# Kernel optimization log

Measured on AMD Instinct MI355X. Metric: run time of the kernel, lower is better.

Reference implementation:

```python
import jax, jax.numpy as jnp
import numpy as np

N = 10000  # num_users + num_posts


def gcn_conv(x, edge_index, W, b):
    """PyG-style GCNConv: out = D^-1/2 (A+I) D^-1/2 (x W) + b."""
    h = x @ W  # [N, d]
    src, dst = edge_index[0], edge_index[1]
    loop = jnp.arange(N, dtype=src.dtype)
    src = jnp.concatenate([src, loop])
    dst = jnp.concatenate([dst, loop])
    ones = jnp.ones(src.shape[0], dtype=h.dtype)
    deg = jax.ops.segment_sum(ones, dst, num_segments=N)  # in-degree incl. self-loop
    dinv = jnp.where(deg > 0, jax.lax.rsqrt(deg), 0.0)
    norm = dinv[src] * dinv[dst]  # [E+N]
    msg = h[src] * norm[:, None]  # gather + scale
    out = jax.ops.segment_sum(msg, dst, num_segments=N)  # scatter-add
    return out + b


def setup_inputs() -> dict:
    key = jax.random.key(0)
    k1, k2, k3, k4 = jax.random.split(key, 4)
    E = 320000
    H = 64
    x = jax.random.normal(k1, (N, N), dtype=jnp.float32)
    edge_index = jax.random.randint(k2, (2, E), 0, N, dtype=jnp.int64)
    W1 = jax.random.normal(k3, (N, H), dtype=jnp.float32) / np.sqrt(N)
    b1 = jnp.zeros((H,), dtype=jnp.float32)
    W2 = jax.random.normal(k4, (H, H), dtype=jnp.float32) / np.sqrt(H)
    b2 = jnp.zeros((H,), dtype=jnp.float32)
    return {"x": x, "edge_index": edge_index, "W1": W1, "b1": b1, "W2": W2, "b2": b2}


def reference(x, edge_index, W1, b1, W2, b2):
    h = gcn_conv(x, edge_index, W1, b1)
    h = jax.nn.relu(h)
    return gcn_conv(h, edge_index, W2, b2)
```

## Files before the change

### kernel.cpp

```cpp
#include <hip/hip_runtime.h>
#include <hip/hip_bf16.h>

#define NND 10000
#define HD 64
#define KPAD 10112
#define ROWS 64
#define RBLK 157
#define NCHUNK 3
#define KCHUNK 3456
#define KSTEP 128
#define KHEAD 5632
#define CAP 96
#define ABYTES 32768
#define BBYTES 16384
#define BUFB (ABYTES + BBYTES)

typedef __attribute__((ext_vector_type(8))) short bf16x8;
typedef __attribute__((ext_vector_type(4))) float f32x4;

__device__ __forceinline__ short f2bf(float f) {
    unsigned u = __builtin_bit_cast(unsigned, f);
    u += 0x7FFFu + ((u >> 16) & 1u);
    return (short)(u >> 16);
}

__device__ __forceinline__ void gload16(const void* gp, void* lp) {
    __builtin_amdgcn_global_load_lds(
        (const __attribute__((address_space(1))) unsigned int*)gp,
        (__attribute__((address_space(3))) unsigned int*)lp, 16, 0, 0);
}

__device__ __forceinline__ void gload16nt(const void* gp, void* lp) {
    __builtin_amdgcn_global_load_lds(
        (const __attribute__((address_space(1))) unsigned int*)gp,
        (__attribute__((address_space(3))) unsigned int*)lp, 16, 0, 2);
}

__global__ __launch_bounds__(256) void prep2_kernel(const float* __restrict__ W1,
        int* __restrict__ cnt, float* __restrict__ h, short* __restrict__ w1t) {
    __shared__ float tile[64][65];
    const int t = threadIdx.x;
    const int k0 = blockIdx.x * 64;
    #pragma unroll
    for (int i = 0; i < 16; ++i) {
        int r = i * 4 + (t >> 6);
        int c = t & 63;
        int k = k0 + r;
        tile[r][c] = (k < NND) ? W1[(size_t)k * HD + c] : 0.f;
    }
    __syncthreads();
    #pragma unroll
    for (int i = 0; i < 16; ++i) {
        int c = i * 4 + (t >> 6);
        int k = t & 63;
        if (k0 + k < KPAD)
            w1t[(size_t)c * KPAD + k0 + k] = f2bf(tile[k][c]);
    }
    int tid = blockIdx.x * 256 + t;
    if (tid < NND) cnt[tid] = 0;
    f32x4* h4 = (f32x4*)h;
    f32x4 z = {0.f, 0.f, 0.f, 0.f};
    #pragma unroll
    for (int i = 0; i < 4; ++i) {
        int idx = tid + i * 40448;
        if (idx < NND * HD / 4) h4[idx] = z;
    }
}

__global__ __launch_bounds__(256, 1) void csrgemm1_kernel(const float* __restrict__ x,
        const short* __restrict__ w1t, float* __restrict__ h,
        const int* __restrict__ ei, int* __restrict__ cnt, int* __restrict__ csr, int E) {
    __shared__ f32x4 smem4[3 * BUFB / 16];
    char* smem = (char*)smem4;
    const int l = threadIdx.x & 63;
    const int w = threadIdx.x >> 6;
    const int r0 = (blockIdx.x / NCHUNK) * ROWS;
    const int kstart = (blockIdx.x % NCHUNK) * KCHUNK;
    const int kend = min(KPAD, kstart + KCHUNK);
    const int nsteps = (kend - kstart) >> 7;

    const int wr = (w & 1) * 32;
    const int wc = (w >> 1) * 32;
    const int akg = l >> 4;
    const int l15 = l & 15;
    const int l7 = l & 7;

    f32x4 acc[2][2];
    #pragma unroll
    for (int i = 0; i < 2; ++i)
        #pragma unroll
        for (int j = 0; j < 2; ++j) acc[i][j] = f32x4{0.f, 0.f, 0.f, 0.f};

    union AFU { bf16x8 v; __hip_bfloat162 p[4]; };

    auto stage = [&](int buf, int k0) {
        char* sb = smem + buf * BUFB;
        const bool cached = (k0 < KHEAD);
        #pragma unroll
        for (int i = 0; i < 8; ++i) {
            int row = w * 16 + i * 2 + (l >> 5);
            int rg = r0 + row; if (rg >= NND) rg = 0;
            int pl = ((l & 31) >> 1) ^ (row & 7);
            const char* gp = (const char*)x + (size_t)rg * (NND * 4)
                             + (size_t)k0 * 4 + pl * 32 + (l & 1) * 16;
            if (k0 + pl * 8 + (l & 1) * 4 + 3 >= NND)
                gp = (const char*)x;
            if (cached) gload16(gp, sb + w * 8192 + i * 1024);
            else        gload16nt(gp, sb + w * 8192 + i * 1024);
        }
        #pragma unroll
        for (int j = 0; j < 4; ++j) {
            int col = w * 16 + j * 4 + (l >> 4);
            int cl = (l & 15) ^ (col & 7);
            const char* gp = (const char*)w1t + (size_t)col * (KPAD * 2)
                             + (size_t)k0 * 2 + cl * 16;
            gload16(gp, sb + ABYTES + w * 4096 + j * 1024);
        }
    };

    stage(0, kstart);
    if (nsteps > 1) stage(1, kstart + KSTEP);
    {
        const int tid = blockIdx.x * 256 + threadIdx.x;
        const int base = tid * 4;
        if (base < E) {
            if (((E & 3) == 0) && base + 4 <= E) {
                int4 sa = *(const int4*)(ei + base);
                int4 da = *(const int4*)(ei + E + base);
                int p0 = atomicAdd(&cnt[da.x], 1);
                int p1 = atomicAdd(&cnt[da.y], 1);
                int p2 = atomicAdd(&cnt[da.z], 1);
                int p3 = atomicAdd(&cnt[da.w], 1);
                if (p0 < CAP) csr[da.x * CAP + p0] = sa.x;
                if (p1 < CAP) csr[da.y * CAP + p1] = sa.y;
                if (p2 < CAP) csr[da.z * CAP + p2] = sa.z;
                if (p3 < CAP) csr[da.w * CAP + p3] = sa.w;
            } else {
                for (int e = base; e < E && e < base + 4; ++e) {
                    int s = ei[e], d = ei[E + e];
                    int pos = atomicAdd(&cnt[d], 1);
                    if (pos < CAP) csr[d * CAP + pos] = s;
                }
            }
        }
    }
    asm volatile("s_waitcnt vmcnt(0)" ::: "memory");
    for (int t = 0; t < nsteps; ++t) {
        if (t + 1 < nsteps) asm volatile("s_waitcnt vmcnt(12)" ::: "memory");
        else                asm volatile("s_waitcnt vmcnt(0)" ::: "memory");
        __builtin_amdgcn_s_barrier();
        if (t + 2 < nsteps) stage((t + 2) % 3, kstart + (t + 2) * KSTEP);
        const char* sb = smem + (t % 3) * BUFB;
        #pragma unroll
        for (int ks = 0; ks < 4; ++ks) {
            int cp = (ks * 4 + akg) ^ l7;
            #pragma unroll
            for (int rg = 0; rg < 2; ++rg) {
                int arow = wr + rg * 16 + l15;
                const char* ap = sb + arow * 512 + cp * 32;
                f32x4 a0 = *(const f32x4*)ap;
                f32x4 a1 = *(const f32x4*)(ap + 16);
                AFU af;
                af.p[0] = __float22bfloat162_rn(float2{a0[0], a0[1]});
                af.p[1] = __float22bfloat162_rn(float2{a0[2], a0[3]});
                af.p[2] = __float22bfloat162_rn(float2{a1[0], a1[1]});
                af.p[3] = __float22bfloat162_rn(float2{a1[2], a1[3]});
                #pragma unroll
                for (int cg = 0; cg < 2; ++cg) {
                    int col = wc + cg * 16 + l15;
                    bf16x8 b = *(const bf16x8*)(sb + ABYTES + col * 256 + cp * 16);
                    acc[rg][cg] = __builtin_amdgcn_mfma_f32_16x16x32_bf16(af.v, b, acc[rg][cg], 0, 0, 0);
                }
            }
        }
    }
    #pragma unroll
    for (int rg = 0; rg < 2; ++rg) {
        const int crow = r0 + wr + rg * 16 + akg * 4;
        #pragma unroll
        for (int cg = 0; cg < 2; ++cg) {
            const int ccol = wc + cg * 16 + l15;
            #pragma unroll
            for (int j = 0; j < 4; ++j) {
                int row = crow + j;
                if (row < NND)
                    unsafeAtomicAdd(&h[(size_t)row * HD + ccol], acc[rg][cg][j]);
            }
        }
    }
}

__global__ __launch_bounds__(256) void agg1g2_kernel(const float* __restrict__ h,
        const int* __restrict__ csr, const int* __restrict__ cnt,
        const float* __restrict__ b1, const float* __restrict__ W2,
        float* __restrict__ h2) {
    __shared__ float w2s[HD * HD];
    __shared__ float rowbuf[4][HD];
    for (int i = threadIdx.x; i < HD * HD; i += 256) w2s[i] = W2[i];
    const int wave = threadIdx.x >> 6, lane = threadIdx.x & 63;
    const int d = blockIdx.x * 4 + wave;
    const int n = min(cnt[d], CAP);
    const float dd = rsqrtf((float)(n + 1));
    float acc = fmaf(h[(size_t)d * HD + lane], dd * dd, b1[lane]);
    const int* row = csr + d * CAP;
    int j = 0;
    for (; j + 8 <= n; j += 8) {
        int s0 = row[j],   s1 = row[j+1], s2 = row[j+2], s3 = row[j+3];
        int s4 = row[j+4], s5 = row[j+5], s6 = row[j+6], s7 = row[j+7];
        acc = fmaf(h[(size_t)s0 * HD + lane], rsqrtf((float)(cnt[s0] + 1)) * dd, acc);
        acc = fmaf(h[(size_t)s1 * HD + lane], rsqrtf((float)(cnt[s1] + 1)) * dd, acc);
        acc = fmaf(h[(size_t)s2 * HD + lane], rsqrtf((float)(cnt[s2] + 1)) * dd, acc);
        acc = fmaf(h[(size_t)s3 * HD + lane], rsqrtf((float)(cnt[s3] + 1)) * dd, acc);
        acc = fmaf(h[(size_t)s4 * HD + lane], rsqrtf((float)(cnt[s4] + 1)) * dd, acc);
        acc = fmaf(h[(size_t)s5 * HD + lane], rsqrtf((float)(cnt[s5] + 1)) * dd, acc);
        acc = fmaf(h[(size_t)s6 * HD + lane], rsqrtf((float)(cnt[s6] + 1)) * dd, acc);
        acc = fmaf(h[(size_t)s7 * HD + lane], rsqrtf((float)(cnt[s7] + 1)) * dd, acc);
    }
    for (; j < n; ++j) {
        int s0 = row[j];
        acc = fmaf(h[(size_t)s0 * HD + lane], rsqrtf((float)(cnt[s0] + 1)) * dd, acc);
    }
    rowbuf[wave][lane] = fmaxf(acc, 0.f);
    __syncthreads();
    float s = 0.f;
    #pragma unroll
    for (int k = 0; k < HD; ++k)
        s = fmaf(rowbuf[wave][k], w2s[k * HD + lane], s);
    h2[(size_t)d * HD + lane] = s;
}

__global__ __launch_bounds__(256) void agg2_kernel(const float* __restrict__ feat,
        const int* __restrict__ csr, const int* __restrict__ cnt,
        const float* __restrict__ bias, float* __restrict__ out) {
    const int wave = threadIdx.x >> 6, lane = threadIdx.x & 63;
    const int d = blockIdx.x * 4 + wave;
    const int n = min(cnt[d], CAP);
    const float dd = rsqrtf((float)(n + 1));
    float acc = fmaf(feat[(size_t)d * HD + lane], dd * dd, bias[lane]);
    const int* row = csr + d * CAP;
    int j = 0;
    for (; j + 8 <= n; j += 8) {
        int s0 = row[j],   s1 = row[j+1], s2 = row[j+2], s3 = row[j+3];
        int s4 = row[j+4], s5 = row[j+5], s6 = row[j+6], s7 = row[j+7];
        acc = fmaf(feat[(size_t)s0 * HD + lane], rsqrtf((float)(cnt[s0] + 1)) * dd, acc);
        acc = fmaf(feat[(size_t)s1 * HD + lane], rsqrtf((float)(cnt[s1] + 1)) * dd, acc);
        acc = fmaf(feat[(size_t)s2 * HD + lane], rsqrtf((float)(cnt[s2] + 1)) * dd, acc);
        acc = fmaf(feat[(size_t)s3 * HD + lane], rsqrtf((float)(cnt[s3] + 1)) * dd, acc);
        acc = fmaf(feat[(size_t)s4 * HD + lane], rsqrtf((float)(cnt[s4] + 1)) * dd, acc);
        acc = fmaf(feat[(size_t)s5 * HD + lane], rsqrtf((float)(cnt[s5] + 1)) * dd, acc);
        acc = fmaf(feat[(size_t)s6 * HD + lane], rsqrtf((float)(cnt[s6] + 1)) * dd, acc);
        acc = fmaf(feat[(size_t)s7 * HD + lane], rsqrtf((float)(cnt[s7] + 1)) * dd, acc);
    }
    for (; j < n; ++j) {
        int s0 = row[j];
        acc = fmaf(feat[(size_t)s0 * HD + lane], rsqrtf((float)(cnt[s0] + 1)) * dd, acc);
    }
    out[(size_t)d * HD + lane] = acc;
}

extern "C" void kernel_launch(void* const* d_in, const int* in_sizes, int n_in,
                              void* d_out, int out_size, void* d_ws, size_t ws_size,
                              hipStream_t stream) {
    const float* x  = (const float*)d_in[0];
    const int*   ei = (const int*)d_in[1];
    const float* W1 = (const float*)d_in[2];
    const float* b1 = (const float*)d_in[3];
    const float* W2 = (const float*)d_in[4];
    const float* b2 = (const float*)d_in[5];
    float* out = (float*)d_out;
    const int E = in_sizes[1] / 2;

    char* ws = (char*)d_ws;
    int*   cnt  = (int*)(ws);
    float* h    = (float*)(ws + 40000);
    float* h2   = (float*)(ws + 2600000);
    short* w1t  = (short*)(ws + 5160000);
    int*   csr  = (int*)(ws + 6454336);

    prep2_kernel<<<158, 256, 0, stream>>>(W1, cnt, h, w1t);
    csrgemm1_kernel<<<RBLK * NCHUNK, 256, 0, stream>>>(x, w1t, h, ei, cnt, csr, E);
    agg1g2_kernel<<<2500, 256, 0, stream>>>(h, csr, cnt, b1, W2, h2);
    agg2_kernel<<<2500, 256, 0, stream>>>(h2, csr, cnt, b2, out);
}
```

Baseline: 138.4 us.

## Fold source-degree normalization into GEMM epilogue and move CSR build to prep

Builds the CSR adjacency and degree counts in the prep kernel, after a memset of the counts. This lets the GEMM epilogue scale each output row of x·W1 by its own inverse-sqrt degree, and the layer-1 aggregation likewise pre-scales h2. Both aggregation kernels then sum pre-scaled neighbor rows using four independent accumulators, with no per-neighbor count gather or rsqrt. In exchange, edge insertion no longer overlaps with the GEMM prologue loads, and there is an extra memset launch.

New measurement: 143.8 us. +3.9%, slower.

```diff
diff --git a/kernel.cpp b/kernel.cpp
--- a/kernel.cpp
+++ b/kernel.cpp
@@ -37,7 +37,8 @@
 }
 
 __global__ __launch_bounds__(256) void prep2_kernel(const float* __restrict__ W1,
-        int* __restrict__ cnt, float* __restrict__ h, short* __restrict__ w1t) {
+        int* __restrict__ cnt, float* __restrict__ h, short* __restrict__ w1t,
+        const int* __restrict__ ei, int* __restrict__ csr, int E) {
     __shared__ float tile[64][65];
     const int t = threadIdx.x;
     const int k0 = blockIdx.x * 64;
@@ -56,8 +57,7 @@
         if (k0 + k < KPAD)
             w1t[(size_t)c * KPAD + k0 + k] = f2bf(tile[k][c]);
     }
-    int tid = blockIdx.x * 256 + t;
-    if (tid < NND) cnt[tid] = 0;
+    const int tid = blockIdx.x * 256 + t;
     f32x4* h4 = (f32x4*)h;
     f32x4 z = {0.f, 0.f, 0.f, 0.f};
     #pragma unroll
@@ -65,11 +65,40 @@
         int idx = tid + i * 40448;
         if (idx < NND * HD / 4) h4[idx] = z;
     }
+    const int base = tid * 8;
+    if (base + 8 <= E) {
+        int4 sa = *(const int4*)(ei + base);
+        int4 sb = *(const int4*)(ei + base + 4);
+        int4 da = *(const int4*)(ei + E + base);
+        int4 db = *(const int4*)(ei + E + base + 4);
+        int p0 = atomicAdd(&cnt[da.x], 1);
+        int p1 = atomicAdd(&cnt[da.y], 1);
+        int p2 = atomicAdd(&cnt[da.z], 1);
+        int p3 = atomicAdd(&cnt[da.w], 1);
+        int p4 = atomicAdd(&cnt[db.x], 1);
+        int p5 = atomicAdd(&cnt[db.y], 1);
+        int p6 = atomicAdd(&cnt[db.z], 1);
+        int p7 = atomicAdd(&cnt[db.w], 1);
+        if (p0 < CAP) csr[da.x * CAP + p0] = sa.x;
+        if (p1 < CAP) csr[da.y * CAP + p1] = sa.y;
+        if (p2 < CAP) csr[da.z * CAP + p2] = sa.z;
+        if (p3 < CAP) csr[da.w * CAP + p3] = sa.w;
+        if (p4 < CAP) csr[db.x * CAP + p4] = sb.x;
+        if (p5 < CAP) csr[db.y * CAP + p5] = sb.y;
+        if (p6 < CAP) csr[db.z * CAP + p6] = sb.z;
+        if (p7 < CAP) csr[db.w * CAP + p7] = sb.w;
+    } else if (base < E) {
+        for (int e = base; e < E; ++e) {
+            int s = ei[e], d = ei[E + e];
+            int pos = atomicAdd(&cnt[d], 1);
+            if (pos < CAP) csr[d * CAP + pos] = s;
+        }
+    }
 }
 
 __global__ __launch_bounds__(256, 1) void csrgemm1_kernel(const float* __restrict__ x,
         const short* __restrict__ w1t, float* __restrict__ h,
-        const int* __restrict__ ei, int* __restrict__ cnt, int* __restrict__ csr, int E) {
+        const int* __restrict__ cnt) {
     __shared__ f32x4 smem4[3 * BUFB / 16];
     char* smem = (char*)smem4;
     const int l = threadIdx.x & 63;
@@ -120,31 +149,6 @@
 
     stage(0, kstart);
     if (nsteps > 1) stage(1, kstart + KSTEP);
-    {
-        const int tid = blockIdx.x * 256 + threadIdx.x;
-        const int base = tid * 4;
-        if (base < E) {
-            if (((E & 3) == 0) && base + 4 <= E) {
-                int4 sa = *(const int4*)(ei + base);
-                int4 da = *(const int4*)(ei + E + base);
-                int p0 = atomicAdd(&cnt[da.x], 1);
-                int p1 = atomicAdd(&cnt[da.y], 1);
-                int p2 = atomicAdd(&cnt[da.z], 1);
-                int p3 = atomicAdd(&cnt[da.w], 1);
-                if (p0 < CAP) csr[da.x * CAP + p0] = sa.x;
-                if (p1 < CAP) csr[da.y * CAP + p1] = sa.y;
-                if (p2 < CAP) csr[da.z * CAP + p2] = sa.z;
-                if (p3 < CAP) csr[da.w * CAP + p3] = sa.w;
-            } else {
-                for (int e = base; e < E && e < base + 4; ++e) {
-                    int s = ei[e], d = ei[E + e];
-                    int pos = atomicAdd(&cnt[d], 1);
-                    if (pos < CAP) csr[d * CAP + pos] = s;
-                }
-            }
-        }
-    }
-    asm volatile("s_waitcnt vmcnt(0)" ::: "memory");
     for (int t = 0; t < nsteps; ++t) {
         if (t + 1 < nsteps) asm volatile("s_waitcnt vmcnt(12)" ::: "memory");
         else                asm volatile("s_waitcnt vmcnt(0)" ::: "memory");
@@ -178,13 +182,15 @@
     for (int rg = 0; rg < 2; ++rg) {
         const int crow = r0 + wr + rg * 16 + akg * 4;
         #pragma unroll
-        for (int cg = 0; cg < 2; ++cg) {
-            const int ccol = wc + cg * 16 + l15;
-            #pragma unroll
-            for (int j = 0; j < 4; ++j) {
-                int row = crow + j;
-                if (row < NND)
-                    unsafeAtomicAdd(&h[(size_t)row * HD + ccol], acc[rg][cg][j]);
+        for (int j = 0; j < 4; ++j) {
+            int row = crow + j;
+            if (row < NND) {
+                float dd = rsqrtf((float)(min(cnt[row], CAP) + 1));
+                #pragma unroll
+                for (int cg = 0; cg < 2; ++cg) {
+                    const int ccol = wc + cg * 16 + l15;
+                    unsafeAtomicAdd(&h[(size_t)row * HD + ccol], acc[rg][cg][j] * dd);
+                }
             }
         }
     }
@@ -201,32 +207,32 @@
     const int d = blockIdx.x * 4 + wave;
     const int n = min(cnt[d], CAP);
     const float dd = rsqrtf((float)(n + 1));
-    float acc = fmaf(h[(size_t)d * HD + lane], dd * dd, b1[lane]);
+    float sA = h[(size_t)d * HD + lane];
+    float sB = 0.f, sC = 0.f, sD = 0.f;
     const int* row = csr + d * CAP;
     int j = 0;
     for (; j + 8 <= n; j += 8) {
-        int s0 = row[j],   s1 = row[j+1], s2 = row[j+2], s3 = row[j+3];
-        int s4 = row[j+4], s5 = row[j+5], s6 = row[j+6], s7 = row[j+7];
-        acc = fmaf(h[(size_t)s0 * HD + lane], rsqrtf((float)(cnt[s0] + 1)) * dd, acc);
-        acc = fmaf(h[(size_t)s1 * HD + lane], rsqrtf((float)(cnt[s1] + 1)) * dd, acc);
-        acc = fmaf(h[(size_t)s2 * HD + lane], rsqrtf((float)(cnt[s2] + 1)) * dd, acc);
-        acc = fmaf(h[(size_t)s3 * HD + lane], rsqrtf((float)(cnt[s3] + 1)) * dd, acc);
-        acc = fmaf(h[(size_t)s4 * HD + lane], rsqrtf((float)(cnt[s4] + 1)) * dd, acc);
-        acc = fmaf(h[(size_t)s5 * HD + lane], rsqrtf((float)(cnt[s5] + 1)) * dd, acc);
-        acc = fmaf(h[(size_t)s6 * HD + lane], rsqrtf((float)(cnt[s6] + 1)) * dd, acc);
-        acc = fmaf(h[(size_t)s7 * HD + lane], rsqrtf((float)(cnt[s7] + 1)) * dd, acc);
-    }
-    for (; j < n; ++j) {
-        int s0 = row[j];
-        acc = fmaf(h[(size_t)s0 * HD + lane], rsqrtf((float)(cnt[s0] + 1)) * dd, acc);
-    }
+        int a0 = row[j],   a1 = row[j+1], a2 = row[j+2], a3 = row[j+3];
+        int a4 = row[j+4], a5 = row[j+5], a6 = row[j+6], a7 = row[j+7];
+        sA += h[(size_t)a0 * HD + lane];
+        sB += h[(size_t)a1 * HD + lane];
+        sC += h[(size_t)a2 * HD + lane];
+        sD += h[(size_t)a3 * HD + lane];
+        sA += h[(size_t)a4 * HD + lane];
+        sB += h[(size_t)a5 * HD + lane];
+        sC += h[(size_t)a6 * HD + lane];
+        sD += h[(size_t)a7 * HD + lane];
+    }
+    for (; j < n; ++j) sA += h[(size_t)row[j] * HD + lane];
+    float sum = (sA + sB) + (sC + sD);
+    float acc = fmaf(sum, dd, b1[lane]);
     rowbuf[wave][lane] = fmaxf(acc, 0.f);
     __syncthreads();
     float s = 0.f;
     #pragma unroll
     for (int k = 0; k < HD; ++k)
         s = fmaf(rowbuf[wave][k], w2s[k * HD + lane], s);
-    h2[(size_t)d * HD + lane] = s;
+    h2[(size_t)d * HD + lane] = s * dd;
 }
 
 __global__ __launch_bounds__(256) void agg2_kernel(const float* __restrict__ feat,
@@ -236,26 +242,25 @@
     const int d = blockIdx.x * 4 + wave;
     const int n = min(cnt[d], CAP);
     const float dd = rsqrtf((float)(n + 1));
-    float acc = fmaf(feat[(size_t)d * HD + lane], dd * dd, bias[lane]);
+    float sA = feat[(size_t)d * HD + lane];
+    float sB = 0.f, sC = 0.f, sD = 0.f;
     const int* row = csr + d * CAP;
     int j = 0;
     for (; j + 8 <= n; j += 8) {
-        int s0 = row[j],   s1 = row[j+1], s2 = row[j+2], s3 = row[j+3];
-        int s4 = row[j+4], s5 = row[j+5], s6 = row[j+6], s7 = row[j+7];
-        acc = fmaf(feat[(size_t)s0 * HD + lane], rsqrtf((float)(cnt[s0] + 1)) * dd, acc);
-        acc = fmaf(feat[(size_t)s1 * HD + lane], rsqrtf((float)(cnt[s1] + 1)) * dd, acc);
-        acc = fmaf(feat[(size_t)s2 * HD + lane], rsqrtf((float)(cnt[s2] + 1)) * dd, acc);
-        acc = fmaf(feat[(size_t)s3 * HD + lane], rsqrtf((float)(cnt[s3] + 1)) * dd, acc);
-        acc = fmaf(feat[(size_t)s4 * HD + lane], rsqrtf((float)(cnt[s4] + 1)) * dd, acc);
-        acc = fmaf(feat[(size_t)s5 * HD + lane], rsqrtf((float)(cnt[s5] + 1)) * dd, acc);
-        acc = fmaf(feat[(size_t)s6 * HD + lane], rsqrtf((float)(cnt[s6] + 1)) * dd, acc);
-        acc = fmaf(feat[(size_t)s7 * HD + lane], rsqrtf((float)(cnt[s7] + 1)) * dd, acc);
-    }
-    for (; j < n; ++j) {
-        int s0 = row[j];
-        acc = fmaf(feat[(size_t)s0 * HD + lane], rsqrtf((float)(cnt[s0] + 1)) * dd, acc);
-    }
-    out[(size_t)d * HD + lane] = acc;
+        int a0 = row[j],   a1 = row[j+1], a2 = row[j+2], a3 = row[j+3];
+        int a4 = row[j+4], a5 = row[j+5], a6 = row[j+6], a7 = row[j+7];
+        sA += feat[(size_t)a0 * HD + lane];
+        sB += feat[(size_t)a1 * HD + lane];
+        sC += feat[(size_t)a2 * HD + lane];
+        sD += feat[(size_t)a3 * HD + lane];
+        sA += feat[(size_t)a4 * HD + lane];
+        sB += feat[(size_t)a5 * HD + lane];
+        sC += feat[(size_t)a6 * HD + lane];
+        sD += feat[(size_t)a7 * HD + lane];
+    }
+    for (; j < n; ++j) sA += feat[(size_t)row[j] * HD + lane];
+    float sum = (sA + sB) + (sC + sD);
+    out[(size_t)d * HD + lane] = fmaf(sum, dd, bias[lane]);
 }
 
 extern "C" void kernel_launch(void* const* d_in, const int* in_sizes, int n_in,
@@ -277,8 +282,9 @@
     short* w1t  = (short*)(ws + 5160000);
     int*   csr  = (int*)(ws + 6454336);
 
-    prep2_kernel<<<158, 256, 0, stream>>>(W1, cnt, h, w1t);
-    csrgemm1_kernel<<<RBLK * NCHUNK, 256, 0, stream>>>(x, w1t, h, ei, cnt, csr, E);
+    hipMemsetAsync(cnt, 0, NND * sizeof(int), stream);
+    prep2_kernel<<<158, 256, 0, stream>>>(W1, cnt, h, w1t, ei, csr, E);
+    csrgemm1_kernel<<<RBLK * NCHUNK, 256, 0, stream>>>(x, w1t, h, cnt);
     agg1g2_kernel<<<2500, 256, 0, stream>>>(h, csr, cnt, b1, W2, h2);
     agg2_kernel<<<2500, 256, 0, stream>>>(h2, csr, cnt, b2, out);
 }
```
